# Kernel tuning notes

Measured on AMD Instinct MI355X. Metric: run time of the kernel, lower is better.

The kernel has to match this reference:

```python
import jax, jax.numpy as jnp
import numpy as np

E = 128      # n_routed_experts (hardcoded in DS_CONFIG_FOR_NEMOTRON)
I = 1856     # moe_intermediate_size
K = 6        # num_experts_per_tok
H = 512      # config.hidden_size
T = 4096     # flattened tokens (batch*seq)
C = 320      # per-expert capacity; avg load = T*K/E = 192, C=320 makes drops ~impossible


def setup_inputs() -> dict:
    key = jax.random.key(0)
    k1, k2, k3, k4, k5 = jax.random.split(key, 5)
    return {
        "hidden_states": jax.random.normal(k1, (T, H), jnp.float32),
        "top_k_index": jax.random.randint(k2, (T, K), 0, E, jnp.int32),
        "top_k_weights": jax.random.uniform(k3, (T, K), jnp.float32),
        "w_gate_up": jax.random.normal(k4, (E, H, 2 * I), jnp.float32) * 0.02,
        "w_down": jax.random.normal(k5, (E, I, H), jnp.float32) * 0.02,
    }


def reference(hidden_states, top_k_index, top_k_weights, w_gate_up, w_down):
    # Grouped-GEMM formulation of the naive per-expert loop: sort the (token, k)
    # pairs by expert, pack each expert's tokens into a fixed-capacity buffer,
    # run batched gate/up/down GEMMs over all experts at once, then weighted
    # scatter-add back to token order. Same math as the torch loop.
    N = T * K
    e = top_k_index.reshape(N)                      # expert id per pair
    tok = jnp.repeat(jnp.arange(T), K)              # token id per pair
    w = top_k_weights.reshape(N)

    order = jnp.argsort(e)                          # stable sort by expert
    e_s, tok_s, w_s = e[order], tok[order], w[order]

    counts = jax.ops.segment_sum(jnp.ones((N,), jnp.int32), e, num_segments=E)
    starts = jnp.cumsum(counts) - counts            # exclusive prefix sum
    pos = jnp.arange(N) - starts[e_s]               # rank within expert
    valid = pos < C                                 # capacity guard (never trips at this load)
    slot = jnp.where(valid, e_s * C + pos, E * C)   # overflow -> dummy slot

    # Dispatch: [E*C+1, H] buffer of gathered token states (dummy row absorbs overflow)
    buf = jnp.zeros((E * C + 1, H), hidden_states.dtype).at[slot].set(hidden_states[tok_s])
    x = buf[: E * C].reshape(E, C, H)

    gu = jnp.einsum('ech,ehf->ecf', x, w_gate_up)   # [E, C, 2I]
    gate, up = jnp.split(gu, 2, axis=-1)
    inter = jax.nn.silu(gate) * up                  # [E, C, I]
    y = jnp.einsum('eci,eih->ech', inter, w_down).reshape(E * C, H)

    # Combine: gather each pair's expert output, scale by router weight, scatter-add by token
    gather_idx = jnp.where(valid, e_s * C + pos, 0)
    pair_y = y[gather_idx] * jnp.where(valid, w_s, 0.0)[:, None]
    out = jnp.zeros((T, H), hidden_states.dtype).at[tok_s].add(pair_y)
    # use_context_proj=False: context states alias the hidden states
    return (out, out)
```

## Files before the change

kernel.cpp:

```cpp
#include <hip/hip_runtime.h>
#include <hip/hip_bf16.h>
#include <stdint.h>

#define NE 128
#define NI 1856
#define NKK 6
#define NH 512
#define NT 4096
#define CAP 320
#define NPAIR (NT*NKK)
#define LD2I (2*NI)

typedef unsigned short u16;
typedef __attribute__((ext_vector_type(4))) float f32x4;
typedef __attribute__((ext_vector_type(8))) short bf16x8;
typedef __attribute__((ext_vector_type(4))) short s16x4;
typedef const void __attribute__((address_space(1)))* gas1p;
typedef void __attribute__((address_space(3)))* gas3p;

#define SFENCE __builtin_amdgcn_sched_barrier(0)

__device__ __forceinline__ short f2bf(float f) {
  union { __hip_bfloat16 h; short s; } c; c.h = __float2bfloat16(f); return c.s;
}
__device__ __forceinline__ float bf2f(short s) {
  union { float f; unsigned u; } v; v.u = ((unsigned)(u16)s) << 16; return v.f;
}

__device__ __forceinline__ int xcd_logical(int bid, int n) {
  int q = n >> 3, r = n & 7;
  int xcd = bid & 7, j = bid >> 3;
  return xcd * q + (xcd < r ? xcd : r) + j;
}

__global__ void k_route(const int* __restrict__ topk, int* __restrict__ counts,
                        int* __restrict__ slot_of_pair, int* __restrict__ pair_of_slot) {
  int n = blockIdx.x * 256 + threadIdx.x;
  if (n >= NPAIR) return;
  int e = topk[n];
  int p = atomicAdd(&counts[e], 1);
  int s = (p < CAP) ? e * CAP + p : -1;
  slot_of_pair[n] = s;
  if (s >= 0) pair_of_slot[s] = n;
}

__global__ void k_gather(const float* __restrict__ hid, const int* __restrict__ counts,
                         const int* __restrict__ pair_of_slot, u16* __restrict__ xbuf) {
  int t = threadIdx.x;
  int row = blockIdx.x * 2 + (t >> 7);
  int c = t & 127;
  int e = row / CAP, p = row % CAP;
  if (p >= counts[e]) return;
  int n = pair_of_slot[row];
  int tok = n / NKK;
  f32x4 v = *(const f32x4*)(hid + (size_t)tok * NH + c * 4);
  s16x4 o;
  o[0] = f2bf(v[0]); o[1] = f2bf(v[1]); o[2] = f2bf(v[2]); o[3] = f2bf(v[3]);
  *(s16x4*)(xbuf + (size_t)row * NH + c * 4) = o;
}

__global__ __launch_bounds__(512, 4) void k_gemm1(
    const u16* __restrict__ xbuf, const float* __restrict__ wgu,
    const int* __restrict__ counts, u16* __restrict__ inter, int e0, int nblk)
{
  __shared__ __align__(16) char lds[73728];
  int L = xcd_logical(blockIdx.x, nblk);
  int el = L / 58, nt = L % 58;
  int e = e0 + el;
  int cnt = counts[e]; if (cnt > CAP) cnt = CAP;
  int n0 = nt * 32;
  int t = threadIdx.x, w = t >> 6, l = t & 63;
  int wm = w & 3, wn = w >> 2;
  const char* abase = (const char*)(xbuf + (size_t)e * CAP * NH);

  int bks = l >> 4;
  int c4 = (l & 15) * 4;
  int gcol = (c4 < 32) ? (n0 + c4) : (NI + n0 + (c4 - 32));
  const float* bsrc = wgu + (size_t)e * NH * LD2I + gcol;

  int kg = l >> 4;
  int kg16 = kg * 16;
  int colg = wn * 16 + (l & 15);

  for (int base = 0; base < cnt; base += 256) {
    __syncthreads();

    auto STAGE = [&](int buf, int kt) {
      char* ad = lds + buf * 16384;
      #pragma unroll
      for (int i = 0; i < 2; ++i) {
        int seg = i * 8 + w;
        int o = seg * 1024 + l * 16;
        int r = o >> 6, slot = o & 63;
        int grow = base + r; if (grow > CAP - 1) grow = CAP - 1;
        const char* g = abase + (size_t)grow * (NH * 2) + kt * 64 + (slot ^ ((r & 3) << 4));
        __builtin_amdgcn_global_load_lds((gas1p)g, (gas3p)(ad + seg * 1024), 16, 0, 0);
      }
      char* bd = lds + 49152 + buf * 8192;
      {
        int seg = w;
        int k = seg * 4 + bks;
        const char* g = (const char*)(bsrc + (size_t)(kt * 32 + k) * LD2I);
        __builtin_amdgcn_global_load_lds((gas1p)g, (gas3p)(bd + seg * 1024), 16, 0, 0);
      }
    };

    f32x4 acc[4][2];
    #pragma unroll
    for (int f = 0; f < 4; ++f) { acc[f][0] = (f32x4){0,0,0,0}; acc[f][1] = (f32x4){0,0,0,0}; }

    STAGE(0, 0);
    STAGE(1, 1);
    SFENCE; asm volatile("s_waitcnt vmcnt(3) lgkmcnt(0)" ::: "memory"); SFENCE;

    for (int kt = 0; kt < 16; ++kt) {
      SFENCE; __builtin_amdgcn_s_barrier(); SFENCE;
      int sk = (kt + 2 < 16) ? kt + 2 : 15;
      STAGE((kt + 2) % 3, sk);

      const char* ab = lds + (kt % 3) * 16384;
      const char* bb = lds + 49152 + (kt % 3) * 8192;
      bf16x8 bg, bu;
      #pragma unroll
      for (int j = 0; j < 8; ++j) {
        int k = kg * 8 + j;
        bg[j] = f2bf(*(const float*)(bb + k * 256 + colg * 4));
        bu[j] = f2bf(*(const float*)(bb + k * 256 + (colg + 32) * 4));
      }
      #pragma unroll
      for (int mf = 0; mf < 4; ++mf) {
        int r = wm * 64 + mf * 16 + (l & 15);
        bf16x8 af = *(const bf16x8*)(ab + r * 64 + (kg16 ^ ((r & 3) << 4)));
        acc[mf][0] = __builtin_amdgcn_mfma_f32_16x16x32_bf16(af, bg, acc[mf][0], 0, 0, 0);
        acc[mf][1] = __builtin_amdgcn_mfma_f32_16x16x32_bf16(af, bu, acc[mf][1], 0, 0, 0);
      }
      SFENCE; asm volatile("s_waitcnt vmcnt(3) lgkmcnt(0)" ::: "memory"); SFENCE;
    }
    __syncthreads();

    int cl = wn * 16 + (l & 15);
    #pragma unroll
    for (int mf = 0; mf < 4; ++mf) {
      f32x4 g = acc[mf][0], u = acc[mf][1];
      #pragma unroll
      for (int r = 0; r < 4; ++r) {
        float gv = g[r];
        float val = gv / (1.f + __expf(-gv)) * u[r];
        int rl = wm * 64 + mf * 16 + (l >> 4) * 4 + r;
        *(short*)(lds + rl * 64 + ((cl * 2) ^ ((rl & 3) << 4))) = f2bf(val);
      }
    }
    __syncthreads();
    int rmax = cnt - base; if (rmax > 256) rmax = 256;
    u16* obase = inter + (size_t)(el * CAP + base) * NI + n0;
    #pragma unroll
    for (int i = 0; i < 2; ++i) {
      int task = i * 512 + t;
      int r = task >> 2, p = task & 3;
      if (r < rmax) {
        bf16x8 v = *(const bf16x8*)(lds + r * 64 + ((p * 16) ^ ((r & 3) << 4)));
        *(bf16x8*)(obase + (size_t)r * NI + p * 8) = v;
      }
    }
  }
}

__global__ __launch_bounds__(512, 4) void k_gemm2(
    const u16* __restrict__ inter, const float* __restrict__ wdn,
    const int* __restrict__ counts, u16* __restrict__ Y, int e0, int nblk)
{
  __shared__ __align__(16) char lds[73728];
  int L = xcd_logical(blockIdx.x, nblk);
  int el = L / 8, nt = L % 8;
  int e = e0 + el;
  int cnt = counts[e]; if (cnt > CAP) cnt = CAP;
  int n0 = nt * 64;
  int t = threadIdx.x, w = t >> 6, l = t & 63;
  int wm = w & 3, wn = w >> 2;
  const char* abase = (const char*)(inter + (size_t)el * CAP * NI);

  int bks = l >> 4;
  int c4 = (l & 15) * 4;
  const float* bsrc = wdn + (size_t)e * NI * NH + n0 + c4;

  int kg = l >> 4;
  int kg16 = kg * 16;
  int col0 = wn * 32 + (l & 15);

  for (int base = 0; base < cnt; base += 256) {
    __syncthreads();

    auto STAGE = [&](int buf, int kt) {
      char* ad = lds + buf * 16384;
      #pragma unroll
      for (int i = 0; i < 2; ++i) {
        int seg = i * 8 + w;
        int o = seg * 1024 + l * 16;
        int r = o >> 6, slot = o & 63;
        int grow = base + r; if (grow > CAP - 1) grow = CAP - 1;
        const char* g = abase + (size_t)grow * (NI * 2) + kt * 64 + (slot ^ ((r & 3) << 4));
        __builtin_amdgcn_global_load_lds((gas1p)g, (gas3p)(ad + seg * 1024), 16, 0, 0);
      }
      char* bd = lds + 49152 + buf * 8192;
      {
        int seg = w;
        int k = seg * 4 + bks;
        const char* g = (const char*)(bsrc + (size_t)(kt * 32 + k) * NH);
        __builtin_amdgcn_global_load_lds((gas1p)g, (gas3p)(bd + seg * 1024), 16, 0, 0);
      }
    };

    f32x4 acc[4][2];
    #pragma unroll
    for (int f = 0; f < 4; ++f) { acc[f][0] = (f32x4){0,0,0,0}; acc[f][1] = (f32x4){0,0,0,0}; }

    STAGE(0, 0);
    STAGE(1, 1);
    SFENCE; asm volatile("s_waitcnt vmcnt(3) lgkmcnt(0)" ::: "memory"); SFENCE;

    for (int kt = 0; kt < 58; ++kt) {
      SFENCE; __builtin_amdgcn_s_barrier(); SFENCE;
      int sk = (kt + 2 < 58) ? kt + 2 : 57;
      STAGE((kt + 2) % 3, sk);

      const char* ab = lds + (kt % 3) * 16384;
      const char* bb = lds + 49152 + (kt % 3) * 8192;
      bf16x8 b0, b1;
      #pragma unroll
      for (int j = 0; j < 8; ++j) {
        int k = kg * 8 + j;
        b0[j] = f2bf(*(const float*)(bb + k * 256 + col0 * 4));
        b1[j] = f2bf(*(const float*)(bb + k * 256 + (col0 + 16) * 4));
      }
      #pragma unroll
      for (int mf = 0; mf < 4; ++mf) {
        int r = wm * 64 + mf * 16 + (l & 15);
        bf16x8 af = *(const bf16x8*)(ab + r * 64 + (kg16 ^ ((r & 3) << 4)));
        acc[mf][0] = __builtin_amdgcn_mfma_f32_16x16x32_bf16(af, b0, acc[mf][0], 0, 0, 0);
        acc[mf][1] = __builtin_amdgcn_mfma_f32_16x16x32_bf16(af, b1, acc[mf][1], 0, 0, 0);
      }
      SFENCE; asm volatile("s_waitcnt vmcnt(3) lgkmcnt(0)" ::: "memory"); SFENCE;
    }
    __syncthreads();

    #pragma unroll
    for (int mf = 0; mf < 4; ++mf)
      #pragma unroll
      for (int f = 0; f < 2; ++f) {
        f32x4 a = acc[mf][f];
        int cl = wn * 32 + f * 16 + (l & 15);
        #pragma unroll
        for (int r = 0; r < 4; ++r) {
          int rl = wm * 64 + mf * 16 + (l >> 4) * 4 + r;
          *(short*)(lds + rl * 128 + ((cl * 2) ^ ((rl & 7) << 4))) = f2bf(a[r]);
        }
      }
    __syncthreads();
    int rmax = cnt - base; if (rmax > 256) rmax = 256;
    u16* obase = Y + (size_t)(e * CAP + base) * NH + n0;
    #pragma unroll
    for (int i = 0; i < 4; ++i) {
      int task = i * 512 + t;
      int r = task >> 3, p = task & 7;
      if (r < rmax) {
        bf16x8 v = *(const bf16x8*)(lds + r * 128 + ((p * 16) ^ ((r & 7) << 4)));
        *(bf16x8*)(obase + (size_t)r * NH + p * 8) = v;
      }
    }
  }
}

__global__ void k_combine(const int* __restrict__ slot_of_pair, const float* __restrict__ wts,
                          const u16* __restrict__ Y, float* __restrict__ out)
{
  int t = threadIdx.x;
  int tok = blockIdx.x * 2 + (t >> 7);
  int c = t & 127;
  f32x4 a = (f32x4){0.f, 0.f, 0.f, 0.f};
  #pragma unroll
  for (int k = 0; k < NKK; ++k) {
    int n = tok * NKK + k;
    int s = slot_of_pair[n];
    if (s >= 0) {
      float wv = wts[n];
      s16x4 y = *(const s16x4*)(Y + (size_t)s * NH + c * 4);
      a[0] += wv * bf2f(y[0]);
      a[1] += wv * bf2f(y[1]);
      a[2] += wv * bf2f(y[2]);
      a[3] += wv * bf2f(y[3]);
    }
  }
  *(f32x4*)(out + (size_t)tok * NH + c * 4) = a;
  *(f32x4*)(out + (size_t)(NT + tok) * NH + c * 4) = a;
}

extern "C" void kernel_launch(void* const* d_in, const int* in_sizes, int n_in,
                              void* d_out, int out_size, void* d_ws, size_t ws_size,
                              hipStream_t stream) {
  const float* hid  = (const float*)d_in[0];
  const int*   topk = (const int*)d_in[1];
  const float* wts  = (const float*)d_in[2];
  const float* wgu  = (const float*)d_in[3];
  const float* wdn  = (const float*)d_in[4];

  char* ws = (char*)d_ws;
  size_t off = 0;
  auto alloc = [&](size_t sz) { char* p = ws + off; off = (off + sz + 255) & ~(size_t)255; return p; };
  int* counts        = (int*)alloc(NE * 4);
  int* slot_of_pair  = (int*)alloc((size_t)NPAIR * 4);
  int* pair_of_slot  = (int*)alloc((size_t)NE * CAP * 4);
  u16* xbuf          = (u16*)alloc((size_t)NE * CAP * NH * 2);
  u16* Y             = (u16*)alloc((size_t)NE * CAP * NH * 2);
  size_t remain = ws_size > off ? ws_size - off : 0;
  size_t per_e = (size_t)CAP * NI * 2;
  int chunkE = (int)(remain / per_e);
  if (chunkE > NE) chunkE = NE;
  if (chunkE < 1) chunkE = 1;
  u16* inter = (u16*)(ws + off);

  hipMemsetAsync(counts, 0, NE * 4, stream);
  k_route<<<NPAIR / 256, 256, 0, stream>>>(topk, counts, slot_of_pair, pair_of_slot);
  k_gather<<<NE * CAP / 2, 256, 0, stream>>>(hid, counts, pair_of_slot, xbuf);
  for (int e0 = 0; e0 < NE; e0 += chunkE) {
    int ce = NE - e0 < chunkE ? NE - e0 : chunkE;
    int nb1 = ce * 58;
    int nb2 = ce * 8;
    k_gemm1<<<nb1, 512, 0, stream>>>(xbuf, wgu, counts, inter, e0, nb1);
    k_gemm2<<<nb2, 512, 0, stream>>>(inter, wdn, counts, Y, e0, nb2);
  }
  k_combine<<<NT / 2, 256, 0, stream>>>(slot_of_pair, wts, Y, (float*)d_out);
}
```

Before: 571.1 us.

## Split expert GEMM row tiles into separate 128-row blocks with early exit

```diff
diff --git a/kernel.cpp b/kernel.cpp
--- a/kernel.cpp
+++ b/kernel.cpp
@@ -59,18 +59,22 @@
   *(s16x4*)(xbuf + (size_t)row * NH + c * 4) = o;
 }
 
-__global__ __launch_bounds__(512, 4) void k_gemm1(
+__global__ __launch_bounds__(256, 3) void k_gemm1(
     const u16* __restrict__ xbuf, const float* __restrict__ wgu,
     const int* __restrict__ counts, u16* __restrict__ inter, int e0, int nblk)
 {
-  __shared__ __align__(16) char lds[73728];
+  __shared__ __align__(16) char lds[49152];
   int L = xcd_logical(blockIdx.x, nblk);
-  int el = L / 58, nt = L % 58;
+  int el = L / 174;
+  int rem = L % 174;
+  int nt = rem / 3, mt = rem % 3;
   int e = e0 + el;
   int cnt = counts[e]; if (cnt > CAP) cnt = CAP;
+  int row0 = mt * 128;
+  if (row0 >= cnt) return;
   int n0 = nt * 32;
   int t = threadIdx.x, w = t >> 6, l = t & 63;
-  int wm = w & 3, wn = w >> 2;
+  int wm = w >> 1, wn = w & 1;
   const char* abase = (const char*)(xbuf + (size_t)e * CAP * NH);
 
   int bks = l >> 4;
@@ -82,101 +86,102 @@
   int kg16 = kg * 16;
   int colg = wn * 16 + (l & 15);
 
-  for (int base = 0; base < cnt; base += 256) {
-    __syncthreads();
-
-    auto STAGE = [&](int buf, int kt) {
-      char* ad = lds + buf * 16384;
-      #pragma unroll
-      for (int i = 0; i < 2; ++i) {
-        int seg = i * 8 + w;
-        int o = seg * 1024 + l * 16;
-        int r = o >> 6, slot = o & 63;
-        int grow = base + r; if (grow > CAP - 1) grow = CAP - 1;
-        const char* g = abase + (size_t)grow * (NH * 2) + kt * 64 + (slot ^ ((r & 3) << 4));
-        __builtin_amdgcn_global_load_lds((gas1p)g, (gas3p)(ad + seg * 1024), 16, 0, 0);
-      }
-      char* bd = lds + 49152 + buf * 8192;
-      {
-        int seg = w;
-        int k = seg * 4 + bks;
-        const char* g = (const char*)(bsrc + (size_t)(kt * 32 + k) * LD2I);
-        __builtin_amdgcn_global_load_lds((gas1p)g, (gas3p)(bd + seg * 1024), 16, 0, 0);
-      }
-    };
-
-    f32x4 acc[4][2];
-    #pragma unroll
-    for (int f = 0; f < 4; ++f) { acc[f][0] = (f32x4){0,0,0,0}; acc[f][1] = (f32x4){0,0,0,0}; }
-
-    STAGE(0, 0);
-    STAGE(1, 1);
-    SFENCE; asm volatile("s_waitcnt vmcnt(3) lgkmcnt(0)" ::: "memory"); SFENCE;
-
-    for (int kt = 0; kt < 16; ++kt) {
-      SFENCE; __builtin_amdgcn_s_barrier(); SFENCE;
-      int sk = (kt + 2 < 16) ? kt + 2 : 15;
-      STAGE((kt + 2) % 3, sk);
-
-      const char* ab = lds + (kt % 3) * 16384;
-      const char* bb = lds + 49152 + (kt % 3) * 8192;
-      bf16x8 bg, bu;
-      #pragma unroll
-      for (int j = 0; j < 8; ++j) {
-        int k = kg * 8 + j;
-        bg[j] = f2bf(*(const float*)(bb + k * 256 + colg * 4));
-        bu[j] = f2bf(*(const float*)(bb + k * 256 + (colg + 32) * 4));
-      }
-      #pragma unroll
-      for (int mf = 0; mf < 4; ++mf) {
-        int r = wm * 64 + mf * 16 + (l & 15);
-        bf16x8 af = *(const bf16x8*)(ab + r * 64 + (kg16 ^ ((r & 3) << 4)));
-        acc[mf][0] = __builtin_amdgcn_mfma_f32_16x16x32_bf16(af, bg, acc[mf][0], 0, 0, 0);
-        acc[mf][1] = __builtin_amdgcn_mfma_f32_16x16x32_bf16(af, bu, acc[mf][1], 0, 0, 0);
-      }
-      SFENCE; asm volatile("s_waitcnt vmcnt(3) lgkmcnt(0)" ::: "memory"); SFENCE;
-    }
-    __syncthreads();
-
-    int cl = wn * 16 + (l & 15);
+  auto STAGE = [&](int buf, int kt) {
+    char* ad = lds + buf * 8192;
+    #pragma unroll
+    for (int i = 0; i < 2; ++i) {
+      int seg = w * 2 + i;
+      int o = seg * 1024 + l * 16;
+      int r = o >> 6, slot = o & 63;
+      int grow = row0 + r; if (grow > CAP - 1) grow = CAP - 1;
+      const char* g = abase + (size_t)grow * (NH * 2) + kt * 64 + (slot ^ ((r & 3) << 4));
+      __builtin_amdgcn_global_load_lds((gas1p)g, (gas3p)(ad + seg * 1024), 16, 0, 0);
+    }
+    char* bd = lds + 24576 + buf * 8192;
+    #pragma unroll
+    for (int i = 0; i < 2; ++i) {
+      int seg = w * 2 + i;
+      int k = seg * 4 + bks;
+      const char* g = (const char*)(bsrc + (size_t)(kt * 32 + k) * LD2I);
+      __builtin_amdgcn_global_load_lds((gas1p)g, (gas3p)(bd + seg * 1024), 16, 0, 0);
+    }
+  };
+
+  f32x4 acc[4][2];
+  #pragma unroll
+  for (int f = 0; f < 4; ++f) { acc[f][0] = (f32x4){0,0,0,0}; acc[f][1] = (f32x4){0,0,0,0}; }
+
+  STAGE(0, 0);
+  STAGE(1, 1);
+  SFENCE; asm volatile("s_waitcnt vmcnt(4) lgkmcnt(0)" ::: "memory"); SFENCE;
+
+  for (int kt = 0; kt < 16; ++kt) {
+    SFENCE; __builtin_amdgcn_s_barrier(); SFENCE;
+    int sk = (kt + 2 < 16) ? kt + 2 : 15;
+    STAGE((kt + 2) % 3, sk);
+
+    const char* ab = lds + (kt % 3) * 8192;
+    const char* bb = lds + 24576 + (kt % 3) * 8192;
+    bf16x8 bg, bu;
+    #pragma unroll
+    for (int j = 0; j < 8; ++j) {
+      int k = kg * 8 + j;
+      bg[j] = f2bf(*(const float*)(bb + k * 256 + colg * 4));
+      bu[j] = f2bf(*(const float*)(bb + k * 256 + (colg + 32) * 4));
+    }
     #pragma unroll
     for (int mf = 0; mf < 4; ++mf) {
-      f32x4 g = acc[mf][0], u = acc[mf][1];
-      #pragma unroll
-      for (int r = 0; r < 4; ++r) {
-        float gv = g[r];
-        float val = gv / (1.f + __expf(-gv)) * u[r];
-        int rl = wm * 64 + mf * 16 + (l >> 4) * 4 + r;
-        *(short*)(lds + rl * 64 + ((cl * 2) ^ ((rl & 3) << 4))) = f2bf(val);
-      }
-    }
-    __syncthreads();
-    int rmax = cnt - base; if (rmax > 256) rmax = 256;
-    u16* obase = inter + (size_t)(el * CAP + base) * NI + n0;
-    #pragma unroll
-    for (int i = 0; i < 2; ++i) {
-      int task = i * 512 + t;
-      int r = task >> 2, p = task & 3;
-      if (r < rmax) {
-        bf16x8 v = *(const bf16x8*)(lds + r * 64 + ((p * 16) ^ ((r & 3) << 4)));
-        *(bf16x8*)(obase + (size_t)r * NI + p * 8) = v;
-      }
-    }
-  }
-}
-
-__global__ __launch_bounds__(512, 4) void k_gemm2(
+      int r = wm * 64 + mf * 16 + (l & 15);
+      bf16x8 af = *(const bf16x8*)(ab + r * 64 + (kg16 ^ ((r & 3) << 4)));
+      acc[mf][0] = __builtin_amdgcn_mfma_f32_16x16x32_bf16(af, bg, acc[mf][0], 0, 0, 0);
+      acc[mf][1] = __builtin_amdgcn_mfma_f32_16x16x32_bf16(af, bu, acc[mf][1], 0, 0, 0);
+    }
+    SFENCE; asm volatile("s_waitcnt vmcnt(4) lgkmcnt(0)" ::: "memory"); SFENCE;
+  }
+  __syncthreads();
+
+  int cl = wn * 16 + (l & 15);
+  #pragma unroll
+  for (int mf = 0; mf < 4; ++mf) {
+    f32x4 g = acc[mf][0], u = acc[mf][1];
+    #pragma unroll
+    for (int r = 0; r < 4; ++r) {
+      float gv = g[r];
+      float val = gv / (1.f + __expf(-gv)) * u[r];
+      int rl = wm * 64 + mf * 16 + (l >> 4) * 4 + r;
+      *(short*)(lds + rl * 64 + ((cl * 2) ^ ((rl & 3) << 4))) = f2bf(val);
+    }
+  }
+  __syncthreads();
+  int rmax = cnt - row0; if (rmax > 128) rmax = 128;
+  u16* obase = inter + (size_t)(el * CAP + row0) * NI + n0;
+  #pragma unroll
+  for (int i = 0; i < 2; ++i) {
+    int task = i * 256 + t;
+    int r = task >> 2, p = task & 3;
+    if (r < rmax) {
+      bf16x8 v = *(const bf16x8*)(lds + r * 64 + ((p * 16) ^ ((r & 3) << 4)));
+      *(bf16x8*)(obase + (size_t)r * NI + p * 8) = v;
+    }
+  }
+}
+
+__global__ __launch_bounds__(256, 3) void k_gemm2(
     const u16* __restrict__ inter, const float* __restrict__ wdn,
     const int* __restrict__ counts, u16* __restrict__ Y, int e0, int nblk)
 {
-  __shared__ __align__(16) char lds[73728];
+  __shared__ __align__(16) char lds[49152];
   int L = xcd_logical(blockIdx.x, nblk);
-  int el = L / 8, nt = L % 8;
+  int el = L / 24;
+  int rem = L % 24;
+  int nt = rem / 3, mt = rem % 3;
   int e = e0 + el;
   int cnt = counts[e]; if (cnt > CAP) cnt = CAP;
+  int row0 = mt * 128;
+  if (row0 >= cnt) return;
   int n0 = nt * 64;
   int t = threadIdx.x, w = t >> 6, l = t & 63;
-  int wm = w & 3, wn = w >> 2;
+  int wm = w >> 1, wn = w & 1;
   const char* abase = (const char*)(inter + (size_t)el * CAP * NI);
 
   int bks = l >> 4;
@@ -187,85 +192,82 @@
   int kg16 = kg * 16;
   int col0 = wn * 32 + (l & 15);
 
-  for (int base = 0; base < cnt; base += 256) {
-    __syncthreads();
-
-    auto STAGE = [&](int buf, int kt) {
-      char* ad = lds + buf * 16384;
+  auto STAGE = [&](int buf, int kt) {
+    char* ad = lds + buf * 8192;
+    #pragma unroll
+    for (int i = 0; i < 2; ++i) {
+      int seg = w * 2 + i;
+      int o = seg * 1024 + l * 16;
+      int r = o >> 6, slot = o & 63;
+      int grow = row0 + r; if (grow > CAP - 1) grow = CAP - 1;
+      const char* g = abase + (size_t)grow * (NI * 2) + kt * 64 + (slot ^ ((r & 3) << 4));
+      __builtin_amdgcn_global_load_lds((gas1p)g, (gas3p)(ad + seg * 1024), 16, 0, 0);
+    }
+    char* bd = lds + 24576 + buf * 8192;
+    #pragma unroll
+    for (int i = 0; i < 2; ++i) {
+      int seg = w * 2 + i;
+      int k = seg * 4 + bks;
+      const char* g = (const char*)(bsrc + (size_t)(kt * 32 + k) * NH);
+      __builtin_amdgcn_global_load_lds((gas1p)g, (gas3p)(bd + seg * 1024), 16, 0, 0);
+    }
+  };
+
+  f32x4 acc[4][2];
+  #pragma unroll
+  for (int f = 0; f < 4; ++f) { acc[f][0] = (f32x4){0,0,0,0}; acc[f][1] = (f32x4){0,0,0,0}; }
+
+  STAGE(0, 0);
+  STAGE(1, 1);
+  SFENCE; asm volatile("s_waitcnt vmcnt(4) lgkmcnt(0)" ::: "memory"); SFENCE;
+
+  for (int kt = 0; kt < 58; ++kt) {
+    SFENCE; __builtin_amdgcn_s_barrier(); SFENCE;
+    int sk = (kt + 2 < 58) ? kt + 2 : 57;
+    STAGE((kt + 2) % 3, sk);
+
+    const char* ab = lds + (kt % 3) * 8192;
+    const char* bb = lds + 24576 + (kt % 3) * 8192;
+    bf16x8 b0, b1;
+    #pragma unroll
+    for (int j = 0; j < 8; ++j) {
+      int k = kg * 8 + j;
+      b0[j] = f2bf(*(const float*)(bb + k * 256 + col0 * 4));
+      b1[j] = f2bf(*(const float*)(bb + k * 256 + (col0 + 16) * 4));
+    }
+    #pragma unroll
+    for (int mf = 0; mf < 4; ++mf) {
+      int r = wm * 64 + mf * 16 + (l & 15);
+      bf16x8 af = *(const bf16x8*)(ab + r * 64 + (kg16 ^ ((r & 3) << 4)));
+      acc[mf][0] = __builtin_amdgcn_mfma_f32_16x16x32_bf16(af, b0, acc[mf][0], 0, 0, 0);
+      acc[mf][1] = __builtin_amdgcn_mfma_f32_16x16x32_bf16(af, b1, acc[mf][1], 0, 0, 0);
+    }
+    SFENCE; asm volatile("s_waitcnt vmcnt(4) lgkmcnt(0)" ::: "memory"); SFENCE;
+  }
+  __syncthreads();
+
+  #pragma unroll
+  for (int mf = 0; mf < 4; ++mf)
+    #pragma unroll
+    for (int f = 0; f < 2; ++f) {
+      f32x4 a = acc[mf][f];
+      int cl = wn * 32 + f * 16 + (l & 15);
       #pragma unroll
-      for (int i = 0; i < 2; ++i) {
-        int seg = i * 8 + w;
-        int o = seg * 1024 + l * 16;
-        int r = o >> 6, slot = o & 63;
-        int grow = base + r; if (grow > CAP - 1) grow = CAP - 1;
-        const char* g = abase + (size_t)grow * (NI * 2) + kt * 64 + (slot ^ ((r & 3) << 4));
-        __builtin_amdgcn_global_load_lds((gas1p)g, (gas3p)(ad + seg * 1024), 16, 0, 0);
+      for (int r = 0; r < 4; ++r) {
+        int rl = wm * 64 + mf * 16 + (l >> 4) * 4 + r;
+        *(short*)(lds + rl * 128 + ((cl * 2) ^ ((rl & 7) << 4))) = f2bf(a[r]);
       }
-      char* bd = lds + 49152 + buf * 8192;
-      {
-        int seg = w;
-        int k = seg * 4 + bks;
-        const char* g = (const char*)(bsrc + (size_t)(kt * 32 + k) * NH);
-        __builtin_amdgcn_global_load_lds((gas1p)g, (gas3p)(bd + seg * 1024), 16, 0, 0);
-      }
-    };
-
-    f32x4 acc[4][2];
-    #pragma unroll
-    for (int f = 0; f < 4; ++f) { acc[f][0] = (f32x4){0,0,0,0}; acc[f][1] = (f32x4){0,0,0,0}; }
-
-    STAGE(0, 0);
-    STAGE(1, 1);
-    SFENCE; asm volatile("s_waitcnt vmcnt(3) lgkmcnt(0)" ::: "memory"); SFENCE;
-
-    for (int kt = 0; kt < 58; ++kt) {
-      SFENCE; __builtin_amdgcn_s_barrier(); SFENCE;
-      int sk = (kt + 2 < 58) ? kt + 2 : 57;
-      STAGE((kt + 2) % 3, sk);
-
-      const char* ab = lds + (kt % 3) * 16384;
-      const char* bb = lds + 49152 + (kt % 3) * 8192;
-      bf16x8 b0, b1;
-      #pragma unroll
-      for (int j = 0; j < 8; ++j) {
-        int k = kg * 8 + j;
-        b0[j] = f2bf(*(const float*)(bb + k * 256 + col0 * 4));
-        b1[j] = f2bf(*(const float*)(bb + k * 256 + (col0 + 16) * 4));
-      }
-      #pragma unroll
-      for (int mf = 0; mf < 4; ++mf) {
-        int r = wm * 64 + mf * 16 + (l & 15);
-        bf16x8 af = *(const bf16x8*)(ab + r * 64 + (kg16 ^ ((r & 3) << 4)));
-        acc[mf][0] = __builtin_amdgcn_mfma_f32_16x16x32_bf16(af, b0, acc[mf][0], 0, 0, 0);
-        acc[mf][1] = __builtin_amdgcn_mfma_f32_16x16x32_bf16(af, b1, acc[mf][1], 0, 0, 0);
-      }
-      SFENCE; asm volatile("s_waitcnt vmcnt(3) lgkmcnt(0)" ::: "memory"); SFENCE;
-    }
-    __syncthreads();
-
-    #pragma unroll
-    for (int mf = 0; mf < 4; ++mf)
-      #pragma unroll
-      for (int f = 0; f < 2; ++f) {
-        f32x4 a = acc[mf][f];
-        int cl = wn * 32 + f * 16 + (l & 15);
-        #pragma unroll
-        for (int r = 0; r < 4; ++r) {
-          int rl = wm * 64 + mf * 16 + (l >> 4) * 4 + r;
-          *(short*)(lds + rl * 128 + ((cl * 2) ^ ((rl & 7) << 4))) = f2bf(a[r]);
-        }
-      }
-    __syncthreads();
-    int rmax = cnt - base; if (rmax > 256) rmax = 256;
-    u16* obase = Y + (size_t)(e * CAP + base) * NH + n0;
-    #pragma unroll
-    for (int i = 0; i < 4; ++i) {
-      int task = i * 512 + t;
-      int r = task >> 3, p = task & 7;
-      if (r < rmax) {
-        bf16x8 v = *(const bf16x8*)(lds + r * 128 + ((p * 16) ^ ((r & 7) << 4)));
-        *(bf16x8*)(obase + (size_t)r * NH + p * 8) = v;
-      }
+    }
+  __syncthreads();
+  int rmax = cnt - row0; if (rmax > 128) rmax = 128;
+  u16* obase = Y + (size_t)(e * CAP + row0) * NH + n0;
+  #pragma unroll
+  for (int i = 0; i < 4; ++i) {
+    int task = i * 256 + t;
+    int r = task >> 3, p = task & 7;
+    if (r < rmax) {
+      bf16x8 v = *(const bf16x8*)(lds + r * 128 + ((p * 16) ^ ((r & 7) << 4)));
+      *(bf16x8*)(obase + (size_t)r * NH + p * 8) = v;
     }
   }
 }
@@ -323,10 +325,10 @@
   k_gather<<<NE * CAP / 2, 256, 0, stream>>>(hid, counts, pair_of_slot, xbuf);
   for (int e0 = 0; e0 < NE; e0 += chunkE) {
     int ce = NE - e0 < chunkE ? NE - e0 : chunkE;
-    int nb1 = ce * 58;
-    int nb2 = ce * 8;
-    k_gemm1<<<nb1, 512, 0, stream>>>(xbuf, wgu, counts, inter, e0, nb1);
-    k_gemm2<<<nb2, 512, 0, stream>>>(inter, wdn, counts, Y, e0, nb2);
+    int nb1 = ce * 174;
+    int nb2 = ce * 24;
+    k_gemm1<<<nb1, 256, 0, stream>>>(xbuf, wgu, counts, inter, e0, nb1);
+    k_gemm2<<<nb2, 256, 0, stream>>>(inter, wdn, counts, Y, e0, nb2);
   }
   k_combine<<<NT / 2, 256, 0, stream>>>(slot_of_pair, wts, Y, (float*)d_out);
 }
```

After: 618.6 us. 8.3% more time.
